# Performance work log

Measured on AMD Instinct MI355X. Metric: run time of the kernel, lower is better.

## Reference

```python
import jax, jax.numpy as jnp
import numpy as np
from jax import lax

N = 2048    # atoms
K = 16      # knn neighbors -> E = N*K = 32768 edges
H = 128     # latent width
L = 10      # stacked InteractionNetworks
STEPS = 10  # outer simulation iterations


def _rn(key, shape, scale=0.05):
    return scale * jax.random.normal(key, shape, dtype=jnp.float32)


def setup_inputs() -> dict:
    key = jax.random.key(0)
    ks = iter(jax.random.split(key, 40))
    inp = {
        "pos": jax.random.normal(next(ks), (N, 3), dtype=jnp.float32),
        "node_f": jax.random.normal(next(ks), (N, 24), dtype=jnp.float32),
        "mass": jnp.ones((N,), jnp.float32),
        # node encoder MLP(24,128,2,128)
        "nW1": _rn(next(ks), (24, H)), "nb1": _rn(next(ks), (H,)),
        "nW2": _rn(next(ks), (H, H)), "nb2": _rn(next(ks), (H,)),
        # edge encoder MLP(4,128,2,128)
        "eW1": _rn(next(ks), (4, H)), "eb1": _rn(next(ks), (H,)),
        "eW2": _rn(next(ks), (H, H)), "eb2": _rn(next(ks), (H,)),
        # RelationModel per IN: input = 2*dim_obj + dim_rel = 384, 4 Linear layers (ReLU after each)
        "rmW1": _rn(next(ks), (L, 3 * H, H)), "rmb1": _rn(next(ks), (L, H)),
        "rmW2": _rn(next(ks), (L, H, H)), "rmb2": _rn(next(ks), (L, H)),
        "rmW3": _rn(next(ks), (L, H, H)), "rmb3": _rn(next(ks), (L, H)),
        "rmW4": _rn(next(ks), (L, H, H)), "rmb4": _rn(next(ks), (L, H)),
        # ObjectModel per IN: input = dim_obj + dim_eff = 256 -> hidden 128 -> out 128
        "omW1": _rn(next(ks), (L, 2 * H, H)), "omb1": _rn(next(ks), (L, H)),
        "omW2": _rn(next(ks), (L, H, H)), "omb2": _rn(next(ks), (L, H)),
        # decoder MLP(128,128,2,3)
        "dW1": _rn(next(ks), (H, H)), "db1": _rn(next(ks), (H,)),
        "dW2": _rn(next(ks), (H, 3)), "db2": _rn(next(ks), (3,)),
        "k": K,
    }
    return inp


def _mlp2(x, W1, b1, W2, b2):
    return jax.nn.relu(x @ W1 + b1) @ W2 + b2


def _knn_edges(pos, k):
    # knn(P.pos, k): edge_index[:,0] = sender (neighbor), edge_index[:,1] = receiver
    n = pos.shape[0]
    sq = jnp.sum(pos * pos, axis=1)
    d2 = sq[:, None] + sq[None, :] - 2.0 * (pos @ pos.T)   # [N, N]
    d2 = d2 + 1e9 * jnp.eye(n, dtype=pos.dtype)            # exclude self
    _, idx = lax.top_k(-d2, k)                              # [N, k] nearest
    senders = idx.reshape(-1)                               # [E]
    receivers = jnp.repeat(jnp.arange(n), k)                # [E]
    rel = pos[senders] - pos[receivers]
    dist = jnp.linalg.norm(rel, axis=1, keepdims=True)
    ea0 = jnp.concatenate([rel, dist], axis=1)              # [E, 4]
    return senders, receivers, ea0


def _simulate(pos, node_f, mass, nW1, nb1, nW2, nb2, eW1, eb1, eW2, eb2,
              rmW1, rmb1, rmW2, rmb2, rmW3, rmb3, rmW4, rmb4,
              omW1, omb1, omW2, omb2, dW1, db1, dW2, db2, k):
    n = pos.shape[0]
    # G.pos = G.pos + randn * 0.1 ; G.vels = zeros
    pos = pos + 0.1 * jax.random.normal(jax.random.key(42), pos.shape, dtype=pos.dtype)
    vels = jnp.zeros_like(pos)

    stacked = (rmW1, rmb1, rmW2, rmb2, rmW3, rmb3, rmW4, rmb4,
               omW1, omb1, omW2, omb2)

    for _ in range(STEPS):
        senders, receivers, ea0 = _knn_edges(pos, k)

        # encode
        x = _mlp2(node_f, nW1, nb1, nW2, nb2)    # [N, H]
        ea = _mlp2(ea0, eW1, eb1, eW2, eb2)      # [E, H]

        # process: 10 InteractionNetworks. In the original, layer(P.x, P.senders,
        # P.receivers, P.edge_attr) binds rr=senders, rs=receivers, so the
        # one-hot matmuls obj.t()@rr / obj.t()@rs are gathers by sender/receiver,
        # and e @ rr.t() is a scatter-add onto sender nodes.
        def in_step(carry, p):
            xc, eac = carry
            rW1, rb1, rW2, rb2, rW3, rb3, rW4, rb4, oW1, ob1, oW2, ob2 = p
            b = jnp.concatenate([xc[senders], xc[receivers], eac], axis=1)  # [E, 3H]
            h = jax.nn.relu(b @ rW1 + rb1)
            h = jax.nn.relu(h @ rW2 + rb2)
            h = jax.nn.relu(h @ rW3 + rb3)
            e = jax.nn.relu(h @ rW4 + rb4)                                   # [E, H]
            agg = jax.ops.segment_sum(e, senders, num_segments=n)           # e @ rr.T
            a = jnp.concatenate([xc, agg], axis=1)                           # [N, 2H]
            x_new = jax.nn.relu(a @ oW1 + ob1) @ oW2 + ob2                   # [N, H]
            return (x_new, e), None

        (x, ea), _ = lax.scan(jax.checkpoint(in_step), (x, ea), stacked)

        # decode + update
        forces = _mlp2(x, dW1, db1, dW2, db2)    # [N, 3]
        vels = vels + forces / mass[:, None]
        pos = pos + vels
    return pos


def reference(pos, node_f, mass, nW1, nb1, nW2, nb2, eW1, eb1, eW2, eb2,
              rmW1, rmb1, rmW2, rmb2, rmW3, rmb3, rmW4, rmb4,
              omW1, omb1, omW2, omb2, dW1, db1, dW2, db2, k):
    return _simulate(pos, node_f, mass, nW1, nb1, nW2, nb2, eW1, eb1, eW2, eb2,
                     rmW1, rmb1, rmW2, rmb2, rmW3, rmb3, rmW4, rmb4,
                     omW1, omb1, omW2, omb2, dW1, db1, dW2, db2, k)
```

## Files before the change

### kernel.cpp

```cpp
#include <hip/hip_runtime.h>

#define N_ATOMS 2048
#define KNN 16
#define NE (N_ATOMS*KNN)
#define H 128
#define NL 10
#define NSTEPS 10
#define S4B ((size_t)16384)
#define S8B ((size_t)32768)

typedef unsigned short u16;
typedef __attribute__((ext_vector_type(4))) float f32x4;
typedef __attribute__((ext_vector_type(8))) short bf16x8;

__device__ __forceinline__ u16 f2bf(float x){
  unsigned u = __float_as_uint(x);
  return (u16)((u + 0x7FFFu + ((u >> 16) & 1u)) >> 16);
}
__device__ __forceinline__ float bf2f(u16 v){ return __uint_as_float(((unsigned)v) << 16); }

template<int PITCH>
__device__ __forceinline__ bf16x8 ldsB_m8(const u16* s, int e, int k){
  int byte = e*PITCH + (k<<1); byte ^= ((e&7)<<4);
  return *(const bf16x8*)((const char*)s + byte);
}
template<int PITCH>
__device__ __forceinline__ void lds_st16_m8(u16* s, int row, int k, uint4 v){
  int byte = row*PITCH + (k<<1); byte ^= ((row&7)<<4);
  *(uint4*)((char*)s + byte) = v;
}
template<int PITCH>
__device__ __forceinline__ uint4 lds_ld16_m8(const u16* s, int row, int k){
  int byte = row*PITCH + (k<<1); byte ^= ((row&7)<<4);
  return *(const uint4*)((const char*)s + byte);
}
template<int PITCH>
__device__ __forceinline__ void lds_st8_m8(u16* s, int row, int k, uint2 v){
  int byte = row*PITCH + (k<<1); byte ^= ((row&7)<<4);
  *(uint2*)((char*)s + byte) = v;
}

template<int KST, int KS, int ET, int PITCH>
__device__ __forceinline__ void mfma_gemm_m8(const u16* sBh, const u16* sBl,
    const u16* __restrict__ pWh, const u16* __restrict__ pWl,
    int ksbase, int wpair, int rowbase, int lane, f32x4 acc[2][ET]){
  const int er = lane & 15, kg = lane >> 4;
  const size_t base = ((size_t)(wpair*KST + ksbase)*64 + lane)*8;
  #pragma unroll
  for (int ks = 0; ks < KS; ks++){
    const int klds = ks*32 + kg*8;
    bf16x8 bh[ET], bl[ET];
    #pragma unroll
    for (int et = 0; et < ET; et++){
      bh[et] = ldsB_m8<PITCH>(sBh, rowbase + et*16 + er, klds);
      bl[et] = ldsB_m8<PITCH>(sBl, rowbase + et*16 + er, klds);
    }
    #pragma unroll
    for (int nt = 0; nt < 2; nt++){
      const size_t off = base + (size_t)(nt*KST + ks)*512;
      bf16x8 ah = *(const bf16x8*)(pWh + off);
      bf16x8 al = *(const bf16x8*)(pWl + off);
      #pragma unroll
      for (int et = 0; et < ET; et++){
        acc[nt][et] = __builtin_amdgcn_mfma_f32_16x16x32_bf16(ah, bh[et], acc[nt][et], 0, 0, 0);
        acc[nt][et] = __builtin_amdgcn_mfma_f32_16x16x32_bf16(ah, bl[et], acc[nt][et], 0, 0, 0);
        acc[nt][et] = __builtin_amdgcn_mfma_f32_16x16x32_bf16(al, bh[et], acc[nt][et], 0, 0, 0);
      }
    }
  }
}

#define CLR_M8(acc, ET) { _Pragma("unroll") for (int i_=0;i_<2;i_++){ _Pragma("unroll") for (int j_=0;j_<ET;j_++){ \
  acc[i_][j_][0]=0.f; acc[i_][j_][1]=0.f; acc[i_][j_][2]=0.f; acc[i_][j_][3]=0.f; } } }

template<int ET, int PITCH, bool RELU>
__device__ __forceinline__ void epi_lds_m8(f32x4 acc[2][ET], u16* sh, u16* sl,
    int wpair, int rowbase, int lane, const float* __restrict__ bias){
  const int er = lane & 15, g = lane >> 4;
  #pragma unroll
  for (int nt = 0; nt < 2; nt++){
    const int n0 = (wpair + nt)*16 + g*4;
    f32x4 bv = *(const f32x4*)(bias + n0);
    #pragma unroll
    for (int et = 0; et < ET; et++){
      const int e = rowbase + et*16 + er;
      unsigned hw[2], lw[2];
      #pragma unroll
      for (int q = 0; q < 2; q++){
        float v0 = acc[nt][et][2*q]   + bv[2*q];
        float v1 = acc[nt][et][2*q+1] + bv[2*q+1];
        if (RELU){ v0 = fmaxf(v0, 0.f); v1 = fmaxf(v1, 0.f); }
        u16 h0 = f2bf(v0), h1 = f2bf(v1);
        u16 l0 = f2bf(v0 - bf2f(h0)), l1 = f2bf(v1 - bf2f(h1));
        hw[q] = (unsigned)h0 | ((unsigned)h1 << 16);
        lw[q] = (unsigned)l0 | ((unsigned)l1 << 16);
      }
      uint2 hv; hv.x = hw[0]; hv.y = hw[1];
      uint2 lv; lv.x = lw[0]; lv.y = lw[1];
      lds_st8_m8<PITCH>(sh, e, n0, hv);
      lds_st8_m8<PITCH>(sl, e, n0, lv);
    }
  }
}

__global__ __launch_bounds__(256) void pack_w_m8(const float* __restrict__ W,
    u16* __restrict__ ph, u16* __restrict__ pl, int KS, int L, int lstride, int roff){
  int idx = blockIdx.x*256 + threadIdx.x;
  int per = 8*KS*64;
  if (idx >= per*L) return;
  int l = idx / per, r = idx - l*per;
  int lane = r & 63, rest = r >> 6;
  int ks = rest % KS, nt = rest / KS;
  int n = nt*16 + (lane & 15), kb = ks*32 + (lane >> 4)*8;
  const float* src = W + (size_t)l*lstride;
  u16 h8[8], l8[8];
  #pragma unroll
  for (int j = 0; j < 8; j++){
    float v = src[(size_t)(roff + kb + j)*H + n];
    u16 h = f2bf(v);
    h8[j] = h; l8[j] = f2bf(v - bf2f(h));
  }
  size_t off = (size_t)idx*8;
  uint4 hv, lv;
  hv.x = h8[0]|((unsigned)h8[1]<<16); hv.y = h8[2]|((unsigned)h8[3]<<16);
  hv.z = h8[4]|((unsigned)h8[5]<<16); hv.w = h8[6]|((unsigned)h8[7]<<16);
  lv.x = l8[0]|((unsigned)l8[1]<<16); lv.y = l8[2]|((unsigned)l8[3]<<16);
  lv.z = l8[4]|((unsigned)l8[5]<<16); lv.w = l8[6]|((unsigned)l8[7]<<16);
  *(uint4*)(ph + off) = hv;
  *(uint4*)(pl + off) = lv;
}

__device__ __forceinline__ int lds_byte_f_m8(int r, int k4){
  return (((r<<9) + (k4<<2)) ^ (((r>>3)&7)<<4));
}
__device__ __forceinline__ f32x4 lds4r_f_m8(const float* s, int r, int k4){
  return *(const f32x4*)((const char*)s + lds_byte_f_m8(r,k4));
}
__device__ __forceinline__ void lds4w_f_m8(float* s, int r, int k4, f32x4 v){
  *(f32x4*)((char*)s + lds_byte_f_m8(r,k4)) = v;
}
__device__ __forceinline__ float lds1r_f_m8(const float* s, int r, int k){
  return *(const float*)((const char*)s + lds_byte_f_m8(r, k & ~3) + ((k&3)<<2));
}
template<int KD, int RPT>
__device__ __forceinline__ void gemm_f_m8(const float* sA, const float* __restrict__ gW,
                                          int r0, int c0, float acc[RPT][4]){
  #pragma unroll 2
  for (int k4 = 0; k4 < KD; k4 += 4){
    f32x4 a[RPT];
    #pragma unroll
    for (int i=0;i<RPT;i++) a[i] = lds4r_f_m8(sA, r0+i, k4);
    #pragma unroll
    for (int kk=0;kk<4;kk++){
      f32x4 wv = *(const f32x4*)(gW + (size_t)(k4+kk)*H + c0);
      #pragma unroll
      for (int i=0;i<RPT;i++){
        acc[i][0] = fmaf(a[i][kk], wv[0], acc[i][0]);
        acc[i][1] = fmaf(a[i][kk], wv[1], acc[i][1]);
        acc[i][2] = fmaf(a[i][kk], wv[2], acc[i][2]);
        acc[i][3] = fmaf(a[i][kk], wv[3], acc[i][3]);
      }
    }
  }
}

__device__ __forceinline__ unsigned rotl32_m8(unsigned v, int d){ return (v << d) | (v >> (32 - d)); }
__device__ __forceinline__ void tf2x32_m8(unsigned k0, unsigned k1, unsigned x0, unsigned x1,
                                          unsigned* o0, unsigned* o1){
  unsigned ks2 = k0 ^ k1 ^ 0x1BD11BDAu;
  x0 += k0; x1 += k1;
  const int R0[4] = {13,15,26,6}, R1[4] = {17,29,16,24};
#define TFG(R) { for (int i=0;i<4;i++){ x0 += x1; x1 = rotl32_m8(x1,R[i]); x1 ^= x0; } }
  TFG(R0); x0 += k1;  x1 += ks2 + 1u;
  TFG(R1); x0 += ks2; x1 += k0  + 2u;
  TFG(R0); x0 += k0;  x1 += k1  + 3u;
  TFG(R1); x0 += k1;  x1 += ks2 + 4u;
  TFG(R0); x0 += ks2; x1 += k0  + 5u;
#undef TFG
  *o0 = x0; *o1 = x1;
}
__device__ float bits_to_normal_m8(unsigned bits){
  float f = __uint_as_float((bits >> 9) | 0x3F800000u) - 1.0f;
  const float lo = -0.99999994f;
  float u = fmaxf(lo, __fadd_rn(__fmul_rn(f, 2.0f), lo));
  float w = -log1pf(-__fmul_rn(u, u));
  float p;
  if (w < 5.0f){
    w = __fsub_rn(w, 2.5f);
    p = 2.81022636e-08f;
    p = __fadd_rn(__fmul_rn(p,w),  3.43273939e-07f);
    p = __fadd_rn(__fmul_rn(p,w), -3.5233877e-06f);
    p = __fadd_rn(__fmul_rn(p,w), -4.39150654e-06f);
    p = __fadd_rn(__fmul_rn(p,w),  0.00021858087f);
    p = __fadd_rn(__fmul_rn(p,w), -0.00125372503f);
    p = __fadd_rn(__fmul_rn(p,w), -0.00417768164f);
    p = __fadd_rn(__fmul_rn(p,w),  0.246640727f);
    p = __fadd_rn(__fmul_rn(p,w),  1.50140941f);
  } else {
    w = __fsub_rn(sqrtf(w), 3.0f);
    p = -0.000200214257f;
    p = __fadd_rn(__fmul_rn(p,w),  0.000100950558f);
    p = __fadd_rn(__fmul_rn(p,w),  0.00134934322f);
    p = __fadd_rn(__fmul_rn(p,w), -0.00367342844f);
    p = __fadd_rn(__fmul_rn(p,w),  0.00573950773f);
    p = __fadd_rn(__fmul_rn(p,w), -0.0076224613f);
    p = __fadd_rn(__fmul_rn(p,w),  0.00943887047f);
    p = __fadd_rn(__fmul_rn(p,w),  1.00167406f);
    p = __fadd_rn(__fmul_rn(p,w),  2.83297682f);
  }
  return __fmul_rn(1.41421356f, __fmul_rn(p, u));
}
__device__ __forceinline__ unsigned draw_bits_m8(unsigned k1, unsigned k2, int bk, int m, int half){
  unsigned o0, o1;
  if (bk == 0){
    if (m < half){ tf2x32_m8(k1,k2, (unsigned)m, (unsigned)(m+half), &o0,&o1); return o0; }
    else         { tf2x32_m8(k1,k2, (unsigned)(m-half), (unsigned)m, &o0,&o1); return o1; }
  }
  tf2x32_m8(k1,k2, 0u, (unsigned)m, &o0,&o1);
  return (bk==1) ? (o0^o1) : (bk==2) ? o1 : o0;
}
__global__ __launch_bounds__(64) void rng_init_m8(int* flags){
  if (threadIdx.x < 8) flags[threadIdx.x] = 1;
}
__global__ __launch_bounds__(256) void rng_detect_m8(const float* __restrict__ pos_in, int* flags){
  int m = blockIdx.x*256 + threadIdx.x;
  if (m >= N_ATOMS*3) return;
  unsigned a0,a1,b0,b1,f0,f1;
  tf2x32_m8(0u,0u, 0u,40u, &a0,&a1);
  tf2x32_m8(0u,0u, 1u,41u, &b0,&b1);
  tf2x32_m8(0u,0u, 0u,0u,  &f0,&f1);
  float target = pos_in[m];
  #pragma unroll
  for (int v = 0; v < 8; v++){
    unsigned k1 = (v<4)? a0 : f0, k2 = (v<4)? b0 : f1;
    unsigned bits = draw_bits_m8(k1,k2, v&3, m, 3072);
    float z = bits_to_normal_m8(bits);
    if (fabsf(z - target) > 1e-3f) flags[v] = 0;
  }
}
__global__ __launch_bounds__(64) void rng_select_m8(const int* flags, int* sel){
  if (threadIdx.x == 0){
    int s = -1;
    for (int v = 0; v < 8; v++) if (flags[v]){ s = v; break; }
    sel[0] = (s < 0) ? 1 : (s & 3);
  }
}
__global__ __launch_bounds__(256) void perturb_m8(const float* __restrict__ pos,
    const int* __restrict__ sel, float* __restrict__ posw, float* __restrict__ vels){
  int m = blockIdx.x*256 + threadIdx.x;
  if (m >= N_ATOMS*3) return;
  unsigned bits = draw_bits_m8(0u, 42u, sel[0], m, 3072);
  float z = bits_to_normal_m8(bits);
  posw[m] = __fadd_rn(pos[m], __fmul_rn(0.1f, z));
  vels[m] = 0.f;
}

__global__ __launch_bounds__(128) void node_enc_m8(const float* __restrict__ nf,
    const float* __restrict__ W1, const float* __restrict__ b1,
    const float* __restrict__ W2, const float* __restrict__ b2,
    u16* __restrict__ xh, u16* __restrict__ xl){
  __shared__ float s_in[24];
  __shared__ float s_h[128];
  int n = blockIdx.x, t = threadIdx.x;
  if (t < 24) s_in[t] = nf[n*24 + t];
  __syncthreads();
  float a = b1[t];
  #pragma unroll
  for (int k = 0; k < 24; k++) a = fmaf(s_in[k], W1[k*H + t], a);
  s_h[t] = fmaxf(a, 0.f);
  __syncthreads();
  float a2 = b2[t];
  for (int k = 0; k < H; k++) a2 = fmaf(s_h[k], W2[k*H + t], a2);
  u16 h = f2bf(a2);
  xh[(size_t)n*H + t] = h;
  xl[(size_t)n*H + t] = f2bf(a2 - bf2f(h));
}

__global__ __launch_bounds__(256) void pnode_m8(
    const u16* __restrict__ xh, const u16* __restrict__ xl,
    const u16* __restrict__ pah, const u16* __restrict__ pal,
    const u16* __restrict__ pbh, const u16* __restrict__ pbl,
    float* __restrict__ P1g, float* __restrict__ P2g){
  __shared__ __align__(16) u16 sXh[16*128];
  __shared__ __align__(16) u16 sXl[16*128];
  const int t = threadIdx.x, n0b = blockIdx.x*16;
  const int i = t>>4, seg = t&15;
  {
    uint4 hv = *(const uint4*)(xh + (size_t)(n0b+i)*H + seg*8);
    uint4 lv = *(const uint4*)(xl + (size_t)(n0b+i)*H + seg*8);
    lds_st16_m8<256>(sXh, i, seg*8, hv);
    lds_st16_m8<256>(sXl, i, seg*8, lv);
  }
  __syncthreads();
  const int w = t>>6, lane = t&63, er = lane&15, g = lane>>4;
  f32x4 acc[2][1];
  CLR_M8(acc, 1);
  mfma_gemm_m8<4,4,1,256>(sXh, sXl, pah, pal, 0, w*2, 0, lane, acc);
  #pragma unroll
  for (int nt = 0; nt < 2; nt++)
    *(f32x4*)(P1g + (size_t)(n0b+er)*H + (w*2+nt)*16 + g*4) = acc[nt][0];
  CLR_M8(acc, 1);
  mfma_gemm_m8<4,4,1,256>(sXh, sXl, pbh, pbl, 0, w*2, 0, lane, acc);
  #pragma unroll
  for (int nt = 0; nt < 2; nt++)
    *(f32x4*)(P2g + (size_t)(n0b+er)*H + (w*2+nt)*16 + g*4) = acc[nt][0];
}

__global__ __launch_bounds__(256) void knn_m8(const float* __restrict__ pos,
                                              int* __restrict__ senders,
                                              float* __restrict__ ea0){
  __shared__ float d2[N_ATOMS];
  __shared__ float pv[4];
  __shared__ int   pi[4];
  int r = blockIdx.x, t = threadIdx.x;
  float prx = pos[r*3+0], pry = pos[r*3+1], prz = pos[r*3+2];
  float sqr = __fadd_rn(__fadd_rn(__fmul_rn(prx,prx), __fmul_rn(pry,pry)), __fmul_rn(prz,prz));
  for (int c = t; c < N_ATOMS; c += 256){
    float cx = pos[c*3+0], cy = pos[c*3+1], cz = pos[c*3+2];
    float sqc = __fadd_rn(__fadd_rn(__fmul_rn(cx,cx), __fmul_rn(cy,cy)), __fmul_rn(cz,cz));
    float dot = __fadd_rn(__fadd_rn(__fmul_rn(prx,cx), __fmul_rn(pry,cy)), __fmul_rn(prz,cz));
    float v = __fsub_rn(__fadd_rn(sqr, sqc), __fmul_rn(2.0f, dot));
    d2[c] = (c == r) ? 1e9f : v;
  }
  __syncthreads();
  for (int j = 0; j < KNN; j++){
    float bv = 1e30f; int bi = 0x7fffffff;
    for (int c = t; c < N_ATOMS; c += 256){
      float v = d2[c];
      if (v < bv || (v == bv && c < bi)){ bv = v; bi = c; }
    }
    #pragma unroll
    for (int off = 32; off; off >>= 1){
      float ov = __shfl_down(bv, off);
      int   oi = __shfl_down(bi, off);
      if (ov < bv || (ov == bv && oi < bi)){ bv = ov; bi = oi; }
    }
    if ((t & 63) == 0){ pv[t>>6] = bv; pi[t>>6] = bi; }
    __syncthreads();
    if (t == 0){
      float fv = pv[0]; int fi = pi[0];
      #pragma unroll
      for (int q = 1; q < 4; q++){
        if (pv[q] < fv || (pv[q] == fv && pi[q] < fi)){ fv = pv[q]; fi = pi[q]; }
      }
      senders[r*KNN + j] = fi;
      float dx = __fsub_rn(pos[fi*3+0], prx);
      float dy = __fsub_rn(pos[fi*3+1], pry);
      float dz = __fsub_rn(pos[fi*3+2], prz);
      float ss = __fadd_rn(__fadd_rn(__fmul_rn(dx,dx), __fmul_rn(dy,dy)), __fmul_rn(dz,dz));
      float* o = ea0 + (size_t)(r*KNN + j)*4;
      o[0] = dx; o[1] = dy; o[2] = dz; o[3] = sqrtf(ss);
      d2[fi] = 1e30f;
    }
    __syncthreads();
  }
}

__global__ __launch_bounds__(1024) void csr_build_m8(const int* __restrict__ senders,
    int* __restrict__ rowstart, int* __restrict__ elist){
  __shared__ int cnt[N_ATOMS];
  __shared__ int part[256];
  const int t = threadIdx.x;
  for (int i = t; i < N_ATOMS; i += 1024) cnt[i] = 0;
  __syncthreads();
  #pragma unroll
  for (int k = 0; k < NE/1024; k++){
    int e = t + k*1024;
    atomicAdd(&cnt[senders[e]], 1);
  }
  __syncthreads();
  if (t < 256){
    int base = t*8, s = 0, loc[8];
    #pragma unroll
    for (int i = 0; i < 8; i++){ loc[i] = s; s += cnt[base+i]; }
    part[t] = s;
    __syncthreads();
    if (t == 0){
      int acc = 0;
      for (int i = 0; i < 256; i++){ int v = part[i]; part[i] = acc; acc += v; }
      rowstart[N_ATOMS] = acc;
    }
    __syncthreads();
    int p = part[t];
    #pragma unroll
    for (int i = 0; i < 8; i++){
      int v = p + loc[i];
      rowstart[base+i] = v;
      loc[i] = v;
    }
    __syncthreads();
    #pragma unroll
    for (int i = 0; i < 8; i++) cnt[base+i] = loc[i];
  } else {
    __syncthreads(); __syncthreads(); __syncthreads();
  }
  __syncthreads();
  #pragma unroll
  for (int k = 0; k < NE/1024; k++){
    int e = t + k*1024;
    int slot = atomicAdd(&cnt[senders[e]], 1);
    elist[slot] = e;
  }
  __syncthreads();
  for (int n = t; n < N_ATOMS; n += 1024){
    int b0 = (n == 0) ? 0 : cnt[n-1];
    int e1 = cnt[n];
    for (int i = b0+1; i < e1; i++){
      int v = elist[i]; int j = i-1;
      while (j >= b0 && elist[j] > v){ elist[j+1] = elist[j]; j--; }
      elist[j+1] = v;
    }
  }
}

template<int FIRST>
__global__ __launch_bounds__(256) void chain_m8(
    const float* __restrict__ P1g, const float* __restrict__ P2g,
    u16* __restrict__ eag, const int* __restrict__ senders,
    const float* __restrict__ ea0,
    const float* __restrict__ eW1, const float* __restrict__ eb1,
    const u16* __restrict__ e2h, const u16* __restrict__ e2l, const float* __restrict__ eb2,
    const u16* __restrict__ w1h, const u16* __restrict__ w1l, const float* __restrict__ b1,
    const u16* __restrict__ w2h, const u16* __restrict__ w2l, const float* __restrict__ b2,
    const u16* __restrict__ w3h, const u16* __restrict__ w3l, const float* __restrict__ b3,
    const u16* __restrict__ w4h, const u16* __restrict__ w4l, const float* __restrict__ b4){
  __shared__ __align__(16) u16 sPh[64*128];
  __shared__ __align__(16) u16 sPl[64*128];
  __shared__ __align__(16) u16 sQh[64*128];
  __shared__ __align__(16) u16 sQl[64*128];
  __shared__ float sE0[64*4];
  const int t = threadIdx.x, e0 = blockIdx.x*64;
  const int w = t>>6, lane = t&63, er = lane&15, g = lane>>4;
  const int wpair = w*2;
  f32x4 acc[2][4];
  int sidx[4];
  #pragma unroll
  for (int et = 0; et < 4; et++) sidx[et] = senders[e0 + et*16 + er];
  #pragma unroll
  for (int et = 0; et < 4; et++){
    const int rr = (e0>>4) + et;
    #pragma unroll
    for (int nt = 0; nt < 2; nt++){
      const int n0 = (wpair+nt)*16 + g*4;
      f32x4 p1 = *(const f32x4*)(P1g + (size_t)sidx[et]*H + n0);
      f32x4 p2 = *(const f32x4*)(P2g + (size_t)rr*H + n0);
      acc[nt][et] = p1 + p2;
    }
  }
  if (FIRST){
    if (t < 64){
      uint4 v = *(const uint4*)(ea0 + (size_t)(e0 + t)*4);
      *(uint4*)(sE0 + t*4) = v;
    }
    __syncthreads();
    const int r0e = ((lane>>3)&7)*8, c0e = w*32 + (lane&7)*4;
    f32x4 bv1 = *(const f32x4*)(eb1 + c0e);
    f32x4 w0v = *(const f32x4*)(eW1 + 0*H + c0e);
    f32x4 w1v = *(const f32x4*)(eW1 + 1*H + c0e);
    f32x4 w2v = *(const f32x4*)(eW1 + 2*H + c0e);
    f32x4 w3v = *(const f32x4*)(eW1 + 3*H + c0e);
    #pragma unroll
    for (int i = 0; i < 8; i++){
      int rr = r0e + i;
      float e0v = sE0[rr*4+0], e1v = sE0[rr*4+1], e2v = sE0[rr*4+2], e3v = sE0[rr*4+3];
      unsigned hw[2], lw[2];
      #pragma unroll
      for (int q = 0; q < 2; q++){
        float v0 = fmaf(e3v, w3v[2*q],   fmaf(e2v, w2v[2*q],   fmaf(e1v, w1v[2*q],   fmaf(e0v, w0v[2*q],   bv1[2*q]))));
        float v1 = fmaf(e3v, w3v[2*q+1], fmaf(e2v, w2v[2*q+1], fmaf(e1v, w1v[2*q+1], fmaf(e0v, w0v[2*q+1], bv1[2*q+1]))));
        v0 = fmaxf(v0, 0.f); v1 = fmaxf(v1, 0.f);
        u16 h0 = f2bf(v0), h1 = f2bf(v1);
        u16 l0 = f2bf(v0 - bf2f(h0)), l1 = f2bf(v1 - bf2f(h1));
        hw[q] = (unsigned)h0 | ((unsigned)h1<<16);
        lw[q] = (unsigned)l0 | ((unsigned)l1<<16);
      }
      uint2 hv; hv.x = hw[0]; hv.y = hw[1];
      uint2 lv; lv.x = lw[0]; lv.y = lw[1];
      lds_st8_m8<256>(sQh, rr, c0e, hv);
      lds_st8_m8<256>(sQl, rr, c0e, lv);
    }
    __syncthreads();
    f32x4 acc0[2][4]; CLR_M8(acc0, 4);
    mfma_gemm_m8<4,4,4,256>(sQh, sQl, e2h, e2l, 0, wpair, 0, lane, acc0);
    __syncthreads();
    epi_lds_m8<4,256,false>(acc0, sPh, sPl, wpair, 0, lane, eb2);
    __syncthreads();
  } else {
    const char* src = (const char*)(eag + (size_t)e0*256);
    #pragma unroll
    for (int m = 0; m < 8; m++){
      int byteoff = (t + m*256)*16;
      uint4 v = *(const uint4*)(src + byteoff);
      int row = byteoff>>9, off = byteoff&511;
      lds_st16_m8<256>((off<256)? sPh : sPl, row, (off&255)>>1, v);
    }
    __syncthreads();
  }
  mfma_gemm_m8<4,4,4,256>(sPh, sPl, w1h, w1l, 0, wpair, 0, lane, acc);
  epi_lds_m8<4,256,true>(acc, sQh, sQl, wpair, 0, lane, b1);
  __syncthreads();
  CLR_M8(acc, 4);
  mfma_gemm_m8<4,4,4,256>(sQh, sQl, w2h, w2l, 0, wpair, 0, lane, acc);
  epi_lds_m8<4,256,true>(acc, sPh, sPl, wpair, 0, lane, b2);
  __syncthreads();
  CLR_M8(acc, 4);
  mfma_gemm_m8<4,4,4,256>(sPh, sPl, w3h, w3l, 0, wpair, 0, lane, acc);
  epi_lds_m8<4,256,true>(acc, sQh, sQl, wpair, 0, lane, b3);
  __syncthreads();
  CLR_M8(acc, 4);
  mfma_gemm_m8<4,4,4,256>(sQh, sQl, w4h, w4l, 0, wpair, 0, lane, acc);
  epi_lds_m8<4,256,true>(acc, sPh, sPl, wpair, 0, lane, b4);
  __syncthreads();
  char* dst = (char*)(eag + (size_t)e0*256);
  #pragma unroll
  for (int m = 0; m < 8; m++){
    int byteoff = (t + m*256)*16;
    int row = byteoff>>9, off = byteoff&511;
    uint4 v = lds_ld16_m8<256>((off<256)? sPh : sPl, row, (off&255)>>1);
    *(uint4*)(dst + byteoff) = v;
  }
}

__global__ __launch_bounds__(256) void objagg_m8(
    const u16* __restrict__ xch, const u16* __restrict__ xcl,
    const u16* __restrict__ eag,
    const int* __restrict__ rowstart, const int* __restrict__ elist,
    const u16* __restrict__ o1h, const u16* __restrict__ o1l, const float* __restrict__ ob1,
    const u16* __restrict__ o2h, const u16* __restrict__ o2l, const float* __restrict__ ob2,
    const u16* __restrict__ nah, const u16* __restrict__ nal,
    const u16* __restrict__ nbh, const u16* __restrict__ nbl,
    u16* __restrict__ xoh, u16* __restrict__ xol,
    float* __restrict__ P1g, float* __restrict__ P2g){
  __shared__ __align__(16) u16 sIh[16*256];
  __shared__ __align__(16) u16 sIl[16*256];
  __shared__ __align__(16) u16 sHh[16*128];
  __shared__ __align__(16) u16 sHl[16*128];
  __shared__ __align__(16) u16 sXh[16*128];
  __shared__ __align__(16) u16 sXl[16*128];
  const int t = threadIdx.x, n0b = blockIdx.x*8;
  const int w = t>>6, lane = t&63;
  const int i = t>>5, c0 = (t&31)*4;
  {
    uint2 hv = *(const uint2*)(xch + (size_t)(n0b+i)*H + c0);
    uint2 lv = *(const uint2*)(xcl + (size_t)(n0b+i)*H + c0);
    lds_st8_m8<512>(sIh, i, c0, hv);
    lds_st8_m8<512>(sIl, i, c0, lv);
    float a0 = 0.f, a1 = 0.f, a2 = 0.f, a3 = 0.f;
    const int b0 = rowstart[n0b+i], e1 = rowstart[n0b+i+1];
    for (int p = b0; p < e1; p++){
      const int ed = elist[p];
      uint2 hv2 = *(const uint2*)(eag + (size_t)ed*256 + c0);
      uint2 lv2 = *(const uint2*)(eag + (size_t)ed*256 + 128 + c0);
      a0 += bf2f((u16)(hv2.x & 0xffffu)) + bf2f((u16)(lv2.x & 0xffffu));
      a1 += bf2f((u16)(hv2.x >> 16))     + bf2f((u16)(lv2.x >> 16));
      a2 += bf2f((u16)(hv2.y & 0xffffu)) + bf2f((u16)(lv2.y & 0xffffu));
      a3 += bf2f((u16)(hv2.y >> 16))     + bf2f((u16)(lv2.y >> 16));
    }
    u16 h0 = f2bf(a0), h1 = f2bf(a1), h2 = f2bf(a2), h3 = f2bf(a3);
    u16 l0 = f2bf(a0 - bf2f(h0)), l1 = f2bf(a1 - bf2f(h1));
    u16 l2 = f2bf(a2 - bf2f(h2)), l3 = f2bf(a3 - bf2f(h3));
    uint2 hvo; hvo.x = (unsigned)h0 | ((unsigned)h1<<16); hvo.y = (unsigned)h2 | ((unsigned)h3<<16);
    uint2 lvo; lvo.x = (unsigned)l0 | ((unsigned)l1<<16); lvo.y = (unsigned)l2 | ((unsigned)l3<<16);
    lds_st8_m8<512>(sIh, i, 128 + c0, hvo);
    lds_st8_m8<512>(sIl, i, 128 + c0, lvo);
  }
  __syncthreads();
  f32x4 acc[2][1];
  CLR_M8(acc, 1);
  mfma_gemm_m8<8,8,1,512>(sIh, sIl, o1h, o1l, 0, w*2, 0, lane, acc);
  epi_lds_m8<1,256,true>(acc, sHh, sHl, w*2, 0, lane, ob1);
  __syncthreads();
  CLR_M8(acc, 1);
  mfma_gemm_m8<4,4,1,256>(sHh, sHl, o2h, o2l, 0, w*2, 0, lane, acc);
  epi_lds_m8<1,256,false>(acc, sXh, sXl, w*2, 0, lane, ob2);
  __syncthreads();
  if (t < 128){
    int row = t>>4, seg = t&15;
    uint4 hv = lds_ld16_m8<256>(sXh, row, seg*8);
    uint4 lv = lds_ld16_m8<256>(sXl, row, seg*8);
    *(uint4*)(xoh + (size_t)(n0b+row)*H + seg*8) = hv;
    *(uint4*)(xol + (size_t)(n0b+row)*H + seg*8) = lv;
  }
  const int er = lane&15, g = lane>>4;
  CLR_M8(acc, 1);
  mfma_gemm_m8<4,4,1,256>(sXh, sXl, nah, nal, 0, w*2, 0, lane, acc);
  if (er < 8){
    #pragma unroll
    for (int nt = 0; nt < 2; nt++)
      *(f32x4*)(P1g + (size_t)(n0b+er)*H + (w*2+nt)*16 + g*4) = acc[nt][0];
  }
  CLR_M8(acc, 1);
  mfma_gemm_m8<4,4,1,256>(sXh, sXl, nbh, nbl, 0, w*2, 0, lane, acc);
  if (er < 8){
    #pragma unroll
    for (int nt = 0; nt < 2; nt++)
      *(f32x4*)(P2g + (size_t)(n0b+er)*H + (w*2+nt)*16 + g*4) = acc[nt][0];
  }
}

__global__ __launch_bounds__(256) void decode_m8(
    const u16* __restrict__ xhi, const u16* __restrict__ xlo,
    const float* __restrict__ dW1, const float* __restrict__ db1,
    const float* __restrict__ dW2, const float* __restrict__ db2,
    const float* __restrict__ mass, float* __restrict__ posw, float* __restrict__ vels){
  __shared__ float sX[16*128];
  __shared__ float sY[16*128];
  const int t = threadIdx.x;
  const int n0 = blockIdx.x*16;
  const int w = t>>6, l = t&63;
  const int r0 = ((l>>3)&7)*2, c0 = w*32 + (l&7)*4;
  const int si = t>>4, sg = t&15;
  {
    const u16* ph = xhi + (size_t)(n0+si)*H + sg*8;
    const u16* pl = xlo + (size_t)(n0+si)*H + sg*8;
    uint4 hv = *(const uint4*)ph;
    uint4 lv = *(const uint4*)pl;
    unsigned hw[4] = {hv.x,hv.y,hv.z,hv.w}, lw[4] = {lv.x,lv.y,lv.z,lv.w};
    f32x4 v0, v1;
    #pragma unroll
    for (int m = 0; m < 2; m++){
      v0[2*m]   = bf2f((u16)(hw[m]&0xffffu)) + bf2f((u16)(lw[m]&0xffffu));
      v0[2*m+1] = bf2f((u16)(hw[m]>>16))     + bf2f((u16)(lw[m]>>16));
      v1[2*m]   = bf2f((u16)(hw[m+2]&0xffffu)) + bf2f((u16)(lw[m+2]&0xffffu));
      v1[2*m+1] = bf2f((u16)(hw[m+2]>>16))     + bf2f((u16)(lw[m+2]>>16));
    }
    lds4w_f_m8(sX, si, sg*8, v0);
    lds4w_f_m8(sX, si, sg*8 + 4, v1);
  }
  __syncthreads();
  float acc[2][4];
  #pragma unroll
  for (int i=0;i<2;i++){ acc[i][0]=0.f; acc[i][1]=0.f; acc[i][2]=0.f; acc[i][3]=0.f; }
  gemm_f_m8<128,2>(sX, dW1, r0, c0, acc);
  {
    f32x4 bv = *(const f32x4*)(db1 + c0);
    #pragma unroll
    for (int i=0;i<2;i++){
      f32x4 v;
      #pragma unroll
      for (int j=0;j<4;j++){ float x = acc[i][j] + bv[j]; v[j] = fmaxf(x, 0.f); }
      lds4w_f_m8(sY, r0+i, c0, v);
    }
  }
  __syncthreads();
  if (t < 48){
    int i = t/3, c = t - i*3;
    float a = db2[c];
    for (int k = 0; k < 128; k++) a = fmaf(lds1r_f_m8(sY, i, k), dW2[k*3 + c], a);
    int n = n0 + i;
    float f = a / mass[n];
    float v = vels[n*3 + c] + f;
    vels[n*3 + c] = v;
    posw[n*3 + c] += v;
  }
}

extern "C" void kernel_launch(void* const* d_in, const int* in_sizes, int n_in,
                              void* d_out, int out_size, void* d_ws, size_t ws_size,
                              hipStream_t stream){
  const float* pos   = (const float*)d_in[0];
  const float* nodef = (const float*)d_in[1];
  const float* mass  = (const float*)d_in[2];
  const float* nW1 = (const float*)d_in[3];  const float* nb1 = (const float*)d_in[4];
  const float* nW2 = (const float*)d_in[5];  const float* nb2 = (const float*)d_in[6];
  const float* eW1 = (const float*)d_in[7];  const float* eb1 = (const float*)d_in[8];
  const float* eW2 = (const float*)d_in[9];  const float* eb2 = (const float*)d_in[10];
  const float* rmW1 = (const float*)d_in[11]; const float* rmb1 = (const float*)d_in[12];
  const float* rmW2 = (const float*)d_in[13]; const float* rmb2 = (const float*)d_in[14];
  const float* rmW3 = (const float*)d_in[15]; const float* rmb3 = (const float*)d_in[16];
  const float* rmW4 = (const float*)d_in[17]; const float* rmb4 = (const float*)d_in[18];
  const float* omW1 = (const float*)d_in[19]; const float* omb1 = (const float*)d_in[20];
  const float* omW2 = (const float*)d_in[21]; const float* omb2 = (const float*)d_in[22];
  const float* dW1 = (const float*)d_in[23]; const float* db1 = (const float*)d_in[24];
  const float* dW2 = (const float*)d_in[25]; const float* db2 = (const float*)d_in[26];

  char* wptr = (char*)d_ws;
  auto alloc = [&](size_t bytes)->void*{
    void* p = (void*)wptr; wptr += (bytes + 255) & ~(size_t)255; return p;
  };
  float* posw  = (float*)alloc((size_t)N_ATOMS*3*4);
  float* vels  = (float*)alloc((size_t)N_ATOMS*3*4);
  int*   senders = (int*)alloc((size_t)NE*4);
  float* ea0   = (float*)alloc((size_t)NE*4*4);
  u16* xench = (u16*)alloc((size_t)N_ATOMS*H*2);
  u16* xencl = (u16*)alloc((size_t)N_ATOMS*H*2);
  u16* xAh   = (u16*)alloc((size_t)N_ATOMS*H*2);
  u16* xAl   = (u16*)alloc((size_t)N_ATOMS*H*2);
  u16* xBh   = (u16*)alloc((size_t)N_ATOMS*H*2);
  u16* xBl   = (u16*)alloc((size_t)N_ATOMS*H*2);
  u16* eag   = (u16*)alloc((size_t)NE*256*2);
  float* P1g  = (float*)alloc((size_t)N_ATOMS*H*4);
  float* P2g  = (float*)alloc((size_t)N_ATOMS*H*4);
  float* P01g = (float*)alloc((size_t)N_ATOMS*H*4);
  float* P02g = (float*)alloc((size_t)N_ATOMS*H*4);
  int* rowstart = (int*)alloc((size_t)(N_ATOMS+1)*4);
  int* elist    = (int*)alloc((size_t)NE*4);
  int* rflags   = (int*)alloc(64);
  int* rsel     = (int*)alloc(64);
  u16* p1ah = (u16*)alloc(S4B*NL*2); u16* p1al = (u16*)alloc(S4B*NL*2);
  u16* p1bh = (u16*)alloc(S4B*NL*2); u16* p1bl = (u16*)alloc(S4B*NL*2);
  u16* p1ch = (u16*)alloc(S4B*NL*2); u16* p1cl = (u16*)alloc(S4B*NL*2);
  u16* prm2h = (u16*)alloc(S4B*NL*2); u16* prm2l = (u16*)alloc(S4B*NL*2);
  u16* prm3h = (u16*)alloc(S4B*NL*2); u16* prm3l = (u16*)alloc(S4B*NL*2);
  u16* prm4h = (u16*)alloc(S4B*NL*2); u16* prm4l = (u16*)alloc(S4B*NL*2);
  u16* pom1h = (u16*)alloc(S8B*NL*2); u16* pom1l = (u16*)alloc(S8B*NL*2);
  u16* pom2h = (u16*)alloc(S4B*NL*2); u16* pom2l = (u16*)alloc(S4B*NL*2);
  u16* pe2h  = (u16*)alloc(S4B*2);    u16* pe2l  = (u16*)alloc(S4B*2);

  auto pack = [&](const float* W, u16* ph, u16* pl, int KS, int L, int lstride, int roff){
    int total = L*8*KS*64;
    pack_w_m8<<<(total+255)/256, 256, 0, stream>>>(W, ph, pl, KS, L, lstride, roff);
  };
  pack(rmW1, p1ah, p1al, 4, NL, 384*H, 0);
  pack(rmW1, p1bh, p1bl, 4, NL, 384*H, 128);
  pack(rmW1, p1ch, p1cl, 4, NL, 384*H, 256);
  pack(rmW2, prm2h, prm2l, 4, NL, H*H, 0);
  pack(rmW3, prm3h, prm3l, 4, NL, H*H, 0);
  pack(rmW4, prm4h, prm4l, 4, NL, H*H, 0);
  pack(omW1, pom1h, pom1l, 8, NL, 2*H*H, 0);
  pack(omW2, pom2h, pom2l, 4, NL, H*H, 0);
  pack(eW2,  pe2h,  pe2l,  4, 1,  H*H, 0);

  rng_init_m8<<<1, 64, 0, stream>>>(rflags);
  rng_detect_m8<<<(N_ATOMS*3+255)/256, 256, 0, stream>>>(pos, rflags);
  rng_select_m8<<<1, 64, 0, stream>>>(rflags, rsel);
  perturb_m8<<<(N_ATOMS*3+255)/256, 256, 0, stream>>>(pos, rsel, posw, vels);
  node_enc_m8<<<N_ATOMS, 128, 0, stream>>>(nodef, nW1, nb1, nW2, nb2, xench, xencl);
  pnode_m8<<<N_ATOMS/16, 256, 0, stream>>>(xench, xencl, p1ah, p1al, p1bh, p1bl, P01g, P02g);

  for (int s = 0; s < NSTEPS; s++){
    knn_m8<<<N_ATOMS, 256, 0, stream>>>(posw, senders, ea0);
    csr_build_m8<<<1, 1024, 0, stream>>>(senders, rowstart, elist);

    const u16* xch = xench; const u16* xcl = xencl;
    for (int l = 0; l < NL; l++){
      const float* Pa = (l == 0) ? P01g : P1g;
      const float* Pb = (l == 0) ? P02g : P2g;
      if (l == 0){
        chain_m8<1><<<NE/64, 256, 0, stream>>>(Pa, Pb, eag, senders,
            ea0, eW1, eb1, pe2h, pe2l, eb2,
            p1ch  + (size_t)l*S4B, p1cl  + (size_t)l*S4B, rmb1 + l*H,
            prm2h + (size_t)l*S4B, prm2l + (size_t)l*S4B, rmb2 + l*H,
            prm3h + (size_t)l*S4B, prm3l + (size_t)l*S4B, rmb3 + l*H,
            prm4h + (size_t)l*S4B, prm4l + (size_t)l*S4B, rmb4 + l*H);
      } else {
        chain_m8<0><<<NE/64, 256, 0, stream>>>(Pa, Pb, eag, senders,
            ea0, eW1, eb1, pe2h, pe2l, eb2,
            p1ch  + (size_t)l*S4B, p1cl  + (size_t)l*S4B, rmb1 + l*H,
            prm2h + (size_t)l*S4B, prm2l + (size_t)l*S4B, rmb2 + l*H,
            prm3h + (size_t)l*S4B, prm3l + (size_t)l*S4B, rmb3 + l*H,
            prm4h + (size_t)l*S4B, prm4l + (size_t)l*S4B, rmb4 + l*H);
      }
      u16* xnh = (l & 1) ? xAh : xBh;
      u16* xnl = (l & 1) ? xAl : xBl;
      int lp1 = (l < NL-1) ? (l+1) : l;
      objagg_m8<<<N_ATOMS/8, 256, 0, stream>>>(xch, xcl, eag, rowstart, elist,
          pom1h + (size_t)l*S8B, pom1l + (size_t)l*S8B, omb1 + l*H,
          pom2h + (size_t)l*S4B, pom2l + (size_t)l*S4B, omb2 + l*H,
          p1ah + (size_t)lp1*S4B, p1al + (size_t)lp1*S4B,
          p1bh + (size_t)lp1*S4B, p1bl + (size_t)lp1*S4B,
          xnh, xnl, P1g, P2g);
      xch = xnh; xcl = xnl;
    }
    decode_m8<<<N_ATOMS/16, 256, 0, stream>>>(xch, xcl, dW1, db1, dW2, db2, mass, posw, vels);
  }
  hipMemcpyAsync(d_out, posw, (size_t)N_ATOMS*3*4, hipMemcpyDeviceToDevice, stream);
}
```

Baseline: 5.978 ms.

## Parallelize CSR build with per-chunk counts fused into KNN and stable placement

Replaces the single-block CSR builder, which did atomic histogramming, a serial scan and a per-node insertion sort, with a three-stage scheme. The KNN kernel now accumulates per-chunk sender counts with global atomics. A small scan kernel turns these into row starts and per-chunk offsets, and a 32-block placement kernel writes edges in deterministic order by ranking duplicates within each wavefront, which removes the sort. The cost is an added memset and extra launches per step, plus global atomics inside the KNN kernel.

After: 5.132 ms, median of 2. 1.16x faster.

```diff
diff --git a/kernel.cpp b/kernel.cpp
--- a/kernel.cpp
+++ b/kernel.cpp
@@ -6,6 +6,7 @@
 #define H 128
 #define NL 10
 #define NSTEPS 10
+#define NCHUNK 32
 #define S4B ((size_t)16384)
 #define S8B ((size_t)32768)
 
@@ -306,9 +307,10 @@
     *(f32x4*)(P2g + (size_t)(n0b+er)*H + (w*2+nt)*16 + g*4) = acc[nt][0];
 }
 
-__global__ __launch_bounds__(256) void knn_m8(const float* __restrict__ pos,
+__global__ __launch_bounds__(256) void knn_m9(const float* __restrict__ pos,
                                               int* __restrict__ senders,
-                                              float* __restrict__ ea0){
+                                              float* __restrict__ ea0,
+                                              int* __restrict__ countsC){
   __shared__ float d2[N_ATOMS];
   __shared__ float pv[4];
   __shared__ int   pi[4];
@@ -344,6 +346,7 @@
         if (pv[q] < fv || (pv[q] == fv && pi[q] < fi)){ fv = pv[q]; fi = pi[q]; }
       }
       senders[r*KNN + j] = fi;
+      atomicAdd(&countsC[(r>>6)*N_ATOMS + fi], 1);
       float dx = __fsub_rn(pos[fi*3+0], prx);
       float dy = __fsub_rn(pos[fi*3+1], pry);
       float dz = __fsub_rn(pos[fi*3+2], prz);
@@ -356,60 +359,71 @@
   }
 }
 
-__global__ __launch_bounds__(1024) void csr_build_m8(const int* __restrict__ senders,
-    int* __restrict__ rowstart, int* __restrict__ elist){
-  __shared__ int cnt[N_ATOMS];
+__global__ __launch_bounds__(256) void csr_scan2_m9(int* __restrict__ countsC,
+                                                    int* __restrict__ rowstart){
   __shared__ int part[256];
   const int t = threadIdx.x;
-  for (int i = t; i < N_ATOMS; i += 1024) cnt[i] = 0;
-  __syncthreads();
-  #pragma unroll
-  for (int k = 0; k < NE/1024; k++){
-    int e = t + k*1024;
-    atomicAdd(&cnt[senders[e]], 1);
-  }
-  __syncthreads();
-  if (t < 256){
-    int base = t*8, s = 0, loc[8];
-    #pragma unroll
-    for (int i = 0; i < 8; i++){ loc[i] = s; s += cnt[base+i]; }
-    part[t] = s;
+  const int base = t*8;
+  int loc[8];
+  int ssum = 0;
+  #pragma unroll
+  for (int i = 0; i < 8; i++){
+    int s = base + i;
+    int tv = 0;
+    #pragma unroll
+    for (int c = 0; c < NCHUNK; c++) tv += countsC[c*N_ATOMS + s];
+    loc[i] = ssum; ssum += tv;
+  }
+  part[t] = ssum;
+  __syncthreads();
+  if (t == 0){
+    int acc = 0;
+    for (int i = 0; i < 256; i++){ int v = part[i]; part[i] = acc; acc += v; }
+    rowstart[N_ATOMS] = acc;
+  }
+  __syncthreads();
+  int p = part[t];
+  #pragma unroll
+  for (int i = 0; i < 8; i++){
+    int s = base + i;
+    int rs = p + loc[i];
+    rowstart[s] = rs;
+    int b = rs;
+    #pragma unroll
+    for (int c = 0; c < NCHUNK; c++){
+      int tv = countsC[c*N_ATOMS + s];
+      countsC[c*N_ATOMS + s] = b;
+      b += tv;
+    }
+  }
+}
+
+__global__ __launch_bounds__(1024) void csr_place_m9(const int* __restrict__ senders,
+    const int* __restrict__ countsC, int* __restrict__ elist){
+  __shared__ int cnt[N_ATOMS];
+  __shared__ int sL[1024];
+  const int c = blockIdx.x, t = threadIdx.x;
+  cnt[t] = countsC[c*N_ATOMS + t];
+  cnt[1024 + t] = countsC[c*N_ATOMS + 1024 + t];
+  sL[t] = senders[c*1024 + t];
+  __syncthreads();
+  const int w = t>>6, lane = t&63, wb = w<<6;
+  const int my_s = sL[t];
+  int rank = 0, same = 0;
+  for (int k = 0; k < 64; k++){
+    int sk = sL[wb + k];
+    int eq = (sk == my_s) ? 1 : 0;
+    same += eq;
+    if (k < lane) rank += eq;
+  }
+  #pragma unroll
+  for (int round = 0; round < 16; round++){
+    if (w == round){
+      int bb = cnt[my_s];
+      elist[bb + rank] = c*1024 + t;
+      if (rank == same - 1) cnt[my_s] = bb + same;
+    }
     __syncthreads();
-    if (t == 0){
-      int acc = 0;
-      for (int i = 0; i < 256; i++){ int v = part[i]; part[i] = acc; acc += v; }
-      rowstart[N_ATOMS] = acc;
-    }
-    __syncthreads();
-    int p = part[t];
-    #pragma unroll
-    for (int i = 0; i < 8; i++){
-      int v = p + loc[i];
-      rowstart[base+i] = v;
-      loc[i] = v;
-    }
-    __syncthreads();
-    #pragma unroll
-    for (int i = 0; i < 8; i++) cnt[base+i] = loc[i];
-  } else {
-    __syncthreads(); __syncthreads(); __syncthreads();
-  }
-  __syncthreads();
-  #pragma unroll
-  for (int k = 0; k < NE/1024; k++){
-    int e = t + k*1024;
-    int slot = atomicAdd(&cnt[senders[e]], 1);
-    elist[slot] = e;
-  }
-  __syncthreads();
-  for (int n = t; n < N_ATOMS; n += 1024){
-    int b0 = (n == 0) ? 0 : cnt[n-1];
-    int e1 = cnt[n];
-    for (int i = b0+1; i < e1; i++){
-      int v = elist[i]; int j = i-1;
-      while (j >= b0 && elist[j] > v){ elist[j+1] = elist[j]; j--; }
-      elist[j+1] = v;
-    }
   }
 }
 
@@ -695,6 +709,7 @@
   float* P02g = (float*)alloc((size_t)N_ATOMS*H*4);
   int* rowstart = (int*)alloc((size_t)(N_ATOMS+1)*4);
   int* elist    = (int*)alloc((size_t)NE*4);
+  int* countsC  = (int*)alloc((size_t)NCHUNK*N_ATOMS*4);
   int* rflags   = (int*)alloc(64);
   int* rsel     = (int*)alloc(64);
   u16* p1ah = (u16*)alloc(S4B*NL*2); u16* p1al = (u16*)alloc(S4B*NL*2);
@@ -729,8 +744,10 @@
   pnode_m8<<<N_ATOMS/16, 256, 0, stream>>>(xench, xencl, p1ah, p1al, p1bh, p1bl, P01g, P02g);
 
   for (int s = 0; s < NSTEPS; s++){
-    knn_m8<<<N_ATOMS, 256, 0, stream>>>(posw, senders, ea0);
-    csr_build_m8<<<1, 1024, 0, stream>>>(senders, rowstart, elist);
+    hipMemsetAsync(countsC, 0, (size_t)NCHUNK*N_ATOMS*4, stream);
+    knn_m9<<<N_ATOMS, 256, 0, stream>>>(posw, senders, ea0, countsC);
+    csr_scan2_m9<<<1, 256, 0, stream>>>(countsC, rowstart);
+    csr_place_m9<<<NCHUNK, 1024, 0, stream>>>(senders, countsC, elist);
 
     const u16* xch = xench; const u16* xcl = xencl;
     for (int l = 0; l < NL; l++){
```
